# Optimization experiments

Hardware: AMD Instinct MI355X
Metric: run time of the kernel (lower is better)

The kernel has to match this reference:

```python
import jax, jax.numpy as jnp
import numpy as np

H = 16         # num query heads
KV = 8         # num kv heads
HD = 64        # head_dim
WINDOW = 512   # sliding window size
ROPE_BASE = 10000.0


def rotate_half(x):
    x1, x2 = x[..., : x.shape[-1] // 2], x[..., x.shape[-1] // 2 :]
    return jnp.concatenate((-x2, x1), axis=-1)


def rope_cos_sin(seq_len, dim, dtype):
    inv_freq = 1.0 / (ROPE_BASE ** (jnp.arange(0, dim, 2, dtype=jnp.float32) / dim))
    t = jnp.arange(seq_len, dtype=jnp.float32)
    freqs = jnp.outer(t, inv_freq)              # [S, dim/2]
    emb = jnp.concatenate((freqs, freqs), axis=-1)  # [S, dim]
    return jnp.cos(emb).astype(dtype), jnp.sin(emb).astype(dtype)


def setup_inputs() -> dict:
    key = jax.random.key(0)
    ks = jax.random.split(key, 5)
    B, S, D = 2, 2048, 1024
    std = 0.02
    return {
        "hidden_states": jax.random.normal(ks[0], (B, S, D), dtype=jnp.float32),
        "Wq": jax.random.normal(ks[1], (D, H * HD), dtype=jnp.float32) * std,
        "Wk": jax.random.normal(ks[2], (D, KV * HD), dtype=jnp.float32) * std,
        "Wv": jax.random.normal(ks[3], (D, KV * HD), dtype=jnp.float32) * std,
        "Wo": jax.random.normal(ks[4], (H * HD, D), dtype=jnp.float32) * std,
    }


def reference(hidden_states, Wq, Wk, Wv, Wo):
    B, S, D = hidden_states.shape
    n_rep = H // KV

    q = (hidden_states @ Wq).reshape(B, S, H, HD).transpose(0, 2, 1, 3)   # [B,H,S,hd]
    k = (hidden_states @ Wk).reshape(B, S, KV, HD).transpose(0, 2, 1, 3)  # [B,KV,S,hd]
    v = (hidden_states @ Wv).reshape(B, S, KV, HD).transpose(0, 2, 1, 3)

    cos, sin = rope_cos_sin(S, HD, q.dtype)  # [S,hd]
    cos = cos[None, None]
    sin = sin[None, None]
    q = q * cos + rotate_half(q) * sin
    k = k * cos + rotate_half(k) * sin

    # repeat kv heads for GQA ([:, :, None] expand + reshape == repeat along head axis)
    k = jnp.repeat(k, n_rep, axis=1)  # [B,H,S,hd]
    v = jnp.repeat(v, n_rep, axis=1)

    scores = jnp.einsum("bhqd,bhkd->bhqk", q, k) / jnp.sqrt(jnp.asarray(HD, q.dtype))
    i = jnp.arange(S)[:, None]
    j = jnp.arange(S)[None, :]
    allowed = (j <= i) & (j >= i - WINDOW)  # causal + sliding window
    scores = jnp.where(allowed[None, None], scores, -jnp.inf)

    attn = jax.nn.softmax(scores, axis=-1)
    out = jnp.einsum("bhqk,bhkd->bhqd", attn, v)          # [B,H,S,hd]
    out = out.transpose(0, 2, 1, 3).reshape(B, S, H * HD)  # [B,S,D]
    return out @ Wo
```

## Files before the change

### kernel.cpp

```cpp
#include <hip/hip_runtime.h>
#include <hip/hip_bf16.h>

typedef __attribute__((ext_vector_type(8))) short short8;
typedef __attribute__((ext_vector_type(4))) float f32x4;

#define S_LEN 2048
#define NH 16
#define NKV 8
#define HD 64
#define WIN 512
#define DMODEL 1024
#define LOG2_10000 13.287712379549449f

#define GLOAD16(g, l)                                                        \
    __builtin_amdgcn_global_load_lds(                                        \
        (const __attribute__((address_space(1))) unsigned int*)(g),          \
        (__attribute__((address_space(3))) unsigned int*)(l), 16, 0, 0)

__global__ void cast_bf16_kernel(const float* __restrict__ X,
                                 __hip_bfloat16* __restrict__ Y, int n) {
    int i = (blockIdx.x * 256 + threadIdx.x) * 4;
    if (i + 3 < n) {
        float4 v = *reinterpret_cast<const float4*>(X + i);
        Y[i + 0] = __float2bfloat16(v.x);
        Y[i + 1] = __float2bfloat16(v.y);
        Y[i + 2] = __float2bfloat16(v.z);
        Y[i + 3] = __float2bfloat16(v.w);
    }
}

__global__ void transpose_cast4_kernel(const float* __restrict__ W0,
                                       const float* __restrict__ W1,
                                       const float* __restrict__ W2,
                                       const float* __restrict__ W3,
                                       __hip_bfloat16* __restrict__ WqkvT,
                                       __hip_bfloat16* __restrict__ WoT) {
    __shared__ float tile[32][33];
    const int K = DMODEL;
    const float* W;
    __hip_bfloat16* WT;
    int N;
    switch (blockIdx.z) {
        case 0: W = W0; WT = WqkvT;                          N = 1024; break;
        case 1: W = W1; WT = WqkvT + (size_t)1024 * K;       N = 512;  break;
        case 2: W = W2; WT = WqkvT + (size_t)1536 * K;       N = 512;  break;
        default: W = W3; WT = WoT;                           N = 1024; break;
    }
    if ((int)blockIdx.x * 32 >= N) return;
    int nx = blockIdx.x * 32 + threadIdx.x;
    int k0 = blockIdx.y * 32;
#pragma unroll
    for (int r = 0; r < 4; ++r) {
        int k = k0 + threadIdx.y + r * 8;
        tile[threadIdx.y + r * 8][threadIdx.x] = W[(size_t)k * N + nx];
    }
    __syncthreads();
#pragma unroll
    for (int r = 0; r < 4; ++r) {
        int nn = blockIdx.x * 32 + threadIdx.y + r * 8;
        int kk = k0 + threadIdx.x;
        WT[(size_t)nn * K + kk] = __float2bfloat16(tile[threadIdx.x][threadIdx.y + r * 8]);
    }
}

template <int MODE>
__global__ __launch_bounds__(256) void gemm256_kernel(
    const __hip_bfloat16* __restrict__ A,
    const __hip_bfloat16* __restrict__ BT,
    void* __restrict__ o0, void* __restrict__ o1, void* __restrict__ o2,
    int N, int K) {
    __shared__ __hip_bfloat16 ldsA[128 * 32];
    __shared__ __hip_bfloat16 ldsB[128 * 32];
    const int tx = threadIdx.x;
    const int wave = tx >> 6;
    const int lane = tx & 63;
    const int l16 = lane & 15;
    const int quad = lane >> 4;
    const int col0 = blockIdx.x * 128;
    const int row0 = blockIdx.y * 128;
    const int wrow = (wave >> 1) * 64;
    const int wcol = (wave & 1) * 64;

    f32x4 acc[4][4] = {};

    const int arow = tx >> 2;
    const int kc8 = (tx & 3) * 8;
    const __hip_bfloat16* gA = A + (size_t)(row0 + arow) * K + kc8;
    const __hip_bfloat16* gB = BT + (size_t)(col0 + arow) * K + kc8;
    char* lA = (char*)ldsA + tx * 16;
    char* lB = (char*)ldsB + tx * 16;

    for (int k0 = 0; k0 < K; k0 += 32) {
        GLOAD16(gA + k0, lA);
        GLOAD16(gA + (size_t)64 * K + k0, lA + 4096);
        GLOAD16(gB + k0, lB);
        GLOAD16(gB + (size_t)64 * K + k0, lB + 4096);
        __syncthreads();
        short8 af[4], bf[4];
#pragma unroll
        for (int i = 0; i < 4; ++i) {
            af[i] = *reinterpret_cast<const short8*>(
                ldsA + (wrow + i * 16 + l16) * 32 + quad * 8);
            bf[i] = *reinterpret_cast<const short8*>(
                ldsB + (wcol + i * 16 + l16) * 32 + quad * 8);
        }
#pragma unroll
        for (int mi = 0; mi < 4; ++mi)
#pragma unroll
            for (int ni = 0; ni < 4; ++ni)
                acc[mi][ni] = __builtin_amdgcn_mfma_f32_16x16x32_bf16(
                    af[mi], bf[ni], acc[mi][ni], 0, 0, 0);
        __syncthreads();
    }

    const int rbase = row0 + wrow;
    if (MODE == 0) {
        const int cbaseg = col0 + wcol;
        const bool isQ = (cbaseg < DMODEL);
        const bool isK = (cbaseg >= DMODEL) && (cbaseg < DMODEL + 512);
        if (isQ || isK) {
            float invf[2];
            invf[0] = exp2f(-(float)(l16)      * (LOG2_10000 / 32.0f));
            invf[1] = exp2f(-(float)(16 + l16) * (LOG2_10000 / 32.0f));
#pragma unroll
            for (int mi = 0; mi < 4; ++mi)
#pragma unroll
                for (int r = 0; r < 4; ++r) {
                    int srow = (rbase + mi * 16 + quad * 4 + r) & (S_LEN - 1);
#pragma unroll
                    for (int ni = 0; ni < 2; ++ni) {
                        float ang = (float)srow * invf[ni];
                        float c = __cosf(ang), s = __sinf(ang);
                        float x1 = acc[mi][ni][r], x2 = acc[mi][ni + 2][r];
                        acc[mi][ni][r]     = x1 * c - x2 * s;
                        acc[mi][ni + 2][r] = x2 * c + x1 * s;
                    }
                }
            __hip_bfloat16* Co = (__hip_bfloat16*)(isQ ? o0 : o1);
            int cbase = isQ ? cbaseg : cbaseg - DMODEL;
            int rowstride = isQ ? (NH * HD) : (NKV * HD);
#pragma unroll
            for (int mi = 0; mi < 4; ++mi)
#pragma unroll
                for (int ni = 0; ni < 4; ++ni) {
                    size_t col = cbase + ni * 16 + l16;
#pragma unroll
                    for (int r = 0; r < 4; ++r)
                        Co[(size_t)(rbase + mi * 16 + quad * 4 + r) * rowstride + col] =
                            __float2bfloat16(acc[mi][ni][r]);
                }
        } else {
            __hip_bfloat16* VTo = (__hip_bfloat16*)o2;
            int bb = row0 >> 11;
#pragma unroll
            for (int mi = 0; mi < 4; ++mi) {
                int s = ((rbase + mi * 16 + quad * 4) & (S_LEN - 1));
#pragma unroll
                for (int ni = 0; ni < 4; ++ni) {
                    int colv = cbaseg - 1536 + ni * 16 + l16;
                    int vh = colv >> 6, d = colv & 63;
                    alignas(8) __hip_bfloat16 hv[4];
#pragma unroll
                    for (int r = 0; r < 4; ++r) hv[r] = __float2bfloat16(acc[mi][ni][r]);
                    *reinterpret_cast<ushort4*>(
                        VTo + ((size_t)(bb * NKV + vh) * HD + d) * S_LEN + s) =
                        *reinterpret_cast<ushort4*>(hv);
                }
            }
        }
    } else {
        float* Co = (float*)o0;
#pragma unroll
        for (int mi = 0; mi < 4; ++mi)
#pragma unroll
            for (int ni = 0; ni < 4; ++ni) {
                size_t col = col0 + wcol + ni * 16 + l16;
#pragma unroll
                for (int r = 0; r < 4; ++r)
                    Co[(size_t)(rbase + mi * 16 + quad * 4 + r) * N + col] = acc[mi][ni][r];
            }
    }
}

__global__ __launch_bounds__(256) void attn_mfma_kernel(
    const __hip_bfloat16* __restrict__ Q,
    const __hip_bfloat16* __restrict__ K,
    const __hip_bfloat16* __restrict__ VT,
    __hip_bfloat16* __restrict__ O) {
    __shared__ __hip_bfloat16 ldsK[2][64][64];
    __shared__ __hip_bfloat16 ldsVT[2][64][64];
    __shared__ __hip_bfloat16 ldsP[4][16][80];
    const int tx = threadIdx.x;
    const int wave = tx >> 6;
    const int lane = tx & 63;
    const int l16 = lane & 15;
    const int quad = lane >> 4;
    const int q0 = blockIdx.x * 64;
    const int h = blockIdx.y;
    const int b = blockIdx.z;
    const int kvh = h >> 1;
    const int qi = q0 + wave * 16 + l16;

    short8 aq0, aq1;
    {
        const __hip_bfloat16* qp =
            Q + (size_t)(b * S_LEN + qi) * (NH * HD) + h * HD + quad * 8;
        aq0 = *reinterpret_cast<const short8*>(qp);
        aq1 = *reinterpret_cast<const short8*>(qp + 32);
    }
    f32x4 acc_o[4] = {};
    float m = -1e30f, l = 0.f;
    const float SL2 = 0.125f * 1.4426950408889634f;

    const int s_row = tx >> 3;
    const int s_c8 = (((tx & 7) ^ (s_row & 7))) * 8;
    const int sw = (l16 & 7);
    auto stage = [&](int j0, int bf) {
        char* lk = (char*)(&ldsK[bf][0][0]) + tx * 16;
        char* lv = (char*)(&ldsVT[bf][0][0]) + tx * 16;
#pragma unroll
        for (int r = 0; r < 2; ++r) {
            int row = s_row + r * 32;
            GLOAD16(K + (size_t)(b * S_LEN + j0 + row) * (NKV * HD) + kvh * HD + s_c8,
                    lk + r * 4096);
            GLOAD16(VT + ((size_t)(b * NKV + kvh) * HD + row) * S_LEN + j0 + s_c8,
                    lv + r * 4096);
        }
    };

    const int kstart = (q0 >= WIN) ? (q0 - WIN) : 0;
    stage(kstart, 0);
    int buf = 0;

    for (int j0 = kstart; j0 <= q0; j0 += 64) {
        __syncthreads();
        if (j0 + 64 <= q0) stage(j0 + 64, buf ^ 1);

        f32x4 sacc[4] = {};
#pragma unroll
        for (int t = 0; t < 4; ++t) {
            const __hip_bfloat16* krow = &ldsK[buf][t * 16 + l16][0];
            short8 bk0 = *reinterpret_cast<const short8*>(krow + ((quad ^ sw) * 8));
            short8 bk1 = *reinterpret_cast<const short8*>(krow + (((4 + quad) ^ sw) * 8));
            sacc[t] = __builtin_amdgcn_mfma_f32_16x16x32_bf16(bk0, aq0, sacc[t], 0, 0, 0);
            sacc[t] = __builtin_amdgcn_mfma_f32_16x16x32_bf16(bk1, aq1, sacc[t], 0, 0, 0);
        }

        float sv[4][4];
        const bool need_mask = (j0 == q0) || (q0 >= WIN && j0 == kstart);
        if (need_mask) {
#pragma unroll
            for (int t = 0; t < 4; ++t)
#pragma unroll
                for (int r = 0; r < 4; ++r) {
                    int j = j0 + t * 16 + quad * 4 + r;
                    bool ok = (j <= qi) && (j + WIN >= qi);
                    sv[t][r] = ok ? sacc[t][r] * SL2 : -1e30f;
                }
        } else {
#pragma unroll
            for (int t = 0; t < 4; ++t)
#pragma unroll
                for (int r = 0; r < 4; ++r) sv[t][r] = sacc[t][r] * SL2;
        }

        float cm = -1e30f;
#pragma unroll
        for (int t = 0; t < 4; ++t)
#pragma unroll
            for (int r = 0; r < 4; ++r) cm = fmaxf(cm, sv[t][r]);
        cm = fmaxf(cm, __shfl_xor(cm, 16));
        cm = fmaxf(cm, __shfl_xor(cm, 32));
        float mn = fmaxf(m, cm);
        float alpha = exp2f(m - mn);
        m = mn;
        float sp = 0.f;
#pragma unroll
        for (int t = 0; t < 4; ++t)
#pragma unroll
            for (int r = 0; r < 4; ++r) { sv[t][r] = exp2f(sv[t][r] - mn); sp += sv[t][r]; }
        sp += __shfl_xor(sp, 16);
        sp += __shfl_xor(sp, 32);
        l = l * alpha + sp;
#pragma unroll
        for (int t = 0; t < 4; ++t)
#pragma unroll
            for (int r = 0; r < 4; ++r) acc_o[t][r] *= alpha;

#pragma unroll
        for (int t = 0; t < 4; ++t) {
            alignas(8) __hip_bfloat16 hp[4];
#pragma unroll
            for (int r = 0; r < 4; ++r) hp[r] = __float2bfloat16(sv[t][r]);
            *reinterpret_cast<ushort4*>(&ldsP[wave][l16][t * 16 + quad * 4]) =
                *reinterpret_cast<ushort4*>(hp);
        }
#pragma unroll
        for (int ks = 0; ks < 2; ++ks) {
            short8 pf = *reinterpret_cast<const short8*>(&ldsP[wave][l16][ks * 32 + quad * 8]);
#pragma unroll
            for (int t = 0; t < 4; ++t) {
                const __hip_bfloat16* vrow = &ldsVT[buf][t * 16 + l16][0];
                short8 vf = *reinterpret_cast<const short8*>(
                    vrow + (((ks * 4 + quad) ^ sw) * 8));
                acc_o[t] = __builtin_amdgcn_mfma_f32_16x16x32_bf16(vf, pf, acc_o[t], 0, 0, 0);
            }
        }
        buf ^= 1;
    }

    float inv = 1.f / l;
    __hip_bfloat16* op = O + (size_t)(b * S_LEN + qi) * (NH * HD) + h * HD;
#pragma unroll
    for (int t = 0; t < 4; ++t) {
        alignas(8) __hip_bfloat16 ho[4];
#pragma unroll
        for (int r = 0; r < 4; ++r) ho[r] = __float2bfloat16(acc_o[t][r] * inv);
        *reinterpret_cast<ushort4*>(op + t * 16 + quad * 4) =
            *reinterpret_cast<ushort4*>(ho);
    }
}

extern "C" void kernel_launch(void* const* d_in, const int* in_sizes, int n_in,
                              void* d_out, int out_size, void* d_ws, size_t ws_size,
                              hipStream_t stream) {
    const float* X  = (const float*)d_in[0];
    const float* Wq = (const float*)d_in[1];
    const float* Wk = (const float*)d_in[2];
    const float* Wv = (const float*)d_in[3];
    const float* Wo = (const float*)d_in[4];
    float* out = (float*)d_out;

    const int ROWS = 2 * S_LEN;
    char* ws = (char*)d_ws;
    size_t off = 0;
    __hip_bfloat16* Xb     = (__hip_bfloat16*)(ws + off); off += (size_t)ROWS * DMODEL * 2;
    __hip_bfloat16* WqkvT  = (__hip_bfloat16*)(ws + off); off += (size_t)2048 * DMODEL * 2;
    __hip_bfloat16* WoT    = (__hip_bfloat16*)(ws + off); off += (size_t)DMODEL * DMODEL * 2;
    __hip_bfloat16* Qb     = (__hip_bfloat16*)(ws + off); off += (size_t)ROWS * (NH * HD) * 2;
    __hip_bfloat16* Kb     = (__hip_bfloat16*)(ws + off); off += (size_t)ROWS * (NKV * HD) * 2;
    __hip_bfloat16* VTg    = (__hip_bfloat16*)(ws + off); off += (size_t)ROWS * (NKV * HD) * 2;
    __hip_bfloat16* Ob     = (__hip_bfloat16*)(ws + off); off += (size_t)ROWS * (NH * HD) * 2;

    cast_bf16_kernel<<<(ROWS * DMODEL) / (256 * 4), 256, 0, stream>>>(X, Xb, ROWS * DMODEL);
    transpose_cast4_kernel<<<dim3(32, 32, 4), dim3(32, 8), 0, stream>>>(
        Wq, Wk, Wv, Wo, WqkvT, WoT);

    gemm256_kernel<0><<<dim3(2048 / 128, ROWS / 128), 256, 0, stream>>>(
        Xb, WqkvT, Qb, Kb, VTg, 2048, DMODEL);

    attn_mfma_kernel<<<dim3(S_LEN / 64, NH, 2), 256, 0, stream>>>(Qb, Kb, VTg, Ob);

    gemm256_kernel<1><<<dim3(DMODEL / 128, ROWS / 128), 256, 0, stream>>>(
        Ob, WoT, out, nullptr, nullptr, DMODEL, DMODEL);
}
```

Baseline: 174.7 us.

## Process both GQA query heads per block to share K/V tile loads

Each attention block now handles the two query heads that share one KV head, so each staged K and V^T tile feeds twice the MFMA work. The grid shrinks from 16 to 8 heads along y, halving global K/V traffic and LDS staging per query. It also raises the launch-bounds occupancy hint to 3 blocks per CU. In exchange register pressure roughly doubles for accumulators and Q fragments, the grid has half as many blocks (512), and the larger P scratch buffer uses more LDS.

```diff
diff --git a/kernel.cpp b/kernel.cpp
--- a/kernel.cpp
+++ b/kernel.cpp
@@ -182,34 +182,34 @@
     }
 }
 
-__global__ __launch_bounds__(256) void attn_mfma_kernel(
+__global__ __launch_bounds__(256, 3) void attn_mfma_kernel(
     const __hip_bfloat16* __restrict__ Q,
     const __hip_bfloat16* __restrict__ K,
     const __hip_bfloat16* __restrict__ VT,
     __hip_bfloat16* __restrict__ O) {
     __shared__ __hip_bfloat16 ldsK[2][64][64];
     __shared__ __hip_bfloat16 ldsVT[2][64][64];
-    __shared__ __hip_bfloat16 ldsP[4][16][80];
+    __shared__ __hip_bfloat16 ldsP[4][2][16][80];
     const int tx = threadIdx.x;
     const int wave = tx >> 6;
     const int lane = tx & 63;
     const int l16 = lane & 15;
     const int quad = lane >> 4;
     const int q0 = blockIdx.x * 64;
-    const int h = blockIdx.y;
+    const int kvh = blockIdx.y;
     const int b = blockIdx.z;
-    const int kvh = h >> 1;
     const int qi = q0 + wave * 16 + l16;
 
-    short8 aq0, aq1;
-    {
+    short8 aq[2][2];
+#pragma unroll
+    for (int hh = 0; hh < 2; ++hh) {
         const __hip_bfloat16* qp =
-            Q + (size_t)(b * S_LEN + qi) * (NH * HD) + h * HD + quad * 8;
-        aq0 = *reinterpret_cast<const short8*>(qp);
-        aq1 = *reinterpret_cast<const short8*>(qp + 32);
-    }
-    f32x4 acc_o[4] = {};
-    float m = -1e30f, l = 0.f;
+            Q + (size_t)(b * S_LEN + qi) * (NH * HD) + (2 * kvh + hh) * HD + quad * 8;
+        aq[hh][0] = *reinterpret_cast<const short8*>(qp);
+        aq[hh][1] = *reinterpret_cast<const short8*>(qp + 32);
+    }
+    f32x4 acc_o[2][4] = {};
+    float m[2] = {-1e30f, -1e30f}, l[2] = {0.f, 0.f};
     const float SL2 = 0.125f * 1.4426950408889634f;
 
     const int s_row = tx >> 3;
@@ -236,88 +236,100 @@
         __syncthreads();
         if (j0 + 64 <= q0) stage(j0 + 64, buf ^ 1);
 
-        f32x4 sacc[4] = {};
+        f32x4 sacc[2][4] = {};
 #pragma unroll
         for (int t = 0; t < 4; ++t) {
             const __hip_bfloat16* krow = &ldsK[buf][t * 16 + l16][0];
             short8 bk0 = *reinterpret_cast<const short8*>(krow + ((quad ^ sw) * 8));
             short8 bk1 = *reinterpret_cast<const short8*>(krow + (((4 + quad) ^ sw) * 8));
-            sacc[t] = __builtin_amdgcn_mfma_f32_16x16x32_bf16(bk0, aq0, sacc[t], 0, 0, 0);
-            sacc[t] = __builtin_amdgcn_mfma_f32_16x16x32_bf16(bk1, aq1, sacc[t], 0, 0, 0);
-        }
-
-        float sv[4][4];
+            sacc[0][t] = __builtin_amdgcn_mfma_f32_16x16x32_bf16(bk0, aq[0][0], sacc[0][t], 0, 0, 0);
+            sacc[0][t] = __builtin_amdgcn_mfma_f32_16x16x32_bf16(bk1, aq[0][1], sacc[0][t], 0, 0, 0);
+            sacc[1][t] = __builtin_amdgcn_mfma_f32_16x16x32_bf16(bk0, aq[1][0], sacc[1][t], 0, 0, 0);
+            sacc[1][t] = __builtin_amdgcn_mfma_f32_16x16x32_bf16(bk1, aq[1][1], sacc[1][t], 0, 0, 0);
+        }
+
         const bool need_mask = (j0 == q0) || (q0 >= WIN && j0 == kstart);
-        if (need_mask) {
+#pragma unroll
+        for (int hh = 0; hh < 2; ++hh) {
+            float sv[4][4];
+            if (need_mask) {
+#pragma unroll
+                for (int t = 0; t < 4; ++t)
+#pragma unroll
+                    for (int r = 0; r < 4; ++r) {
+                        int j = j0 + t * 16 + quad * 4 + r;
+                        bool ok = (j <= qi) && (j + WIN >= qi);
+                        sv[t][r] = ok ? sacc[hh][t][r] * SL2 : -1e30f;
+                    }
+            } else {
+#pragma unroll
+                for (int t = 0; t < 4; ++t)
+#pragma unroll
+                    for (int r = 0; r < 4; ++r) sv[t][r] = sacc[hh][t][r] * SL2;
+            }
+            float cm = -1e30f;
 #pragma unroll
             for (int t = 0; t < 4; ++t)
 #pragma unroll
-                for (int r = 0; r < 4; ++r) {
-                    int j = j0 + t * 16 + quad * 4 + r;
-                    bool ok = (j <= qi) && (j + WIN >= qi);
-                    sv[t][r] = ok ? sacc[t][r] * SL2 : -1e30f;
-                }
-        } else {
+                for (int r = 0; r < 4; ++r) cm = fmaxf(cm, sv[t][r]);
+            cm = fmaxf(cm, __shfl_xor(cm, 16));
+            cm = fmaxf(cm, __shfl_xor(cm, 32));
+            float mn = fmaxf(m[hh], cm);
+            float alpha = exp2f(m[hh] - mn);
+            m[hh] = mn;
+            float sp = 0.f;
 #pragma unroll
             for (int t = 0; t < 4; ++t)
 #pragma unroll
-                for (int r = 0; r < 4; ++r) sv[t][r] = sacc[t][r] * SL2;
-        }
-
-        float cm = -1e30f;
-#pragma unroll
-        for (int t = 0; t < 4; ++t)
-#pragma unroll
-            for (int r = 0; r < 4; ++r) cm = fmaxf(cm, sv[t][r]);
-        cm = fmaxf(cm, __shfl_xor(cm, 16));
-        cm = fmaxf(cm, __shfl_xor(cm, 32));
-        float mn = fmaxf(m, cm);
-        float alpha = exp2f(m - mn);
-        m = mn;
-        float sp = 0.f;
-#pragma unroll
-        for (int t = 0; t < 4; ++t)
-#pragma unroll
-            for (int r = 0; r < 4; ++r) { sv[t][r] = exp2f(sv[t][r] - mn); sp += sv[t][r]; }
-        sp += __shfl_xor(sp, 16);
-        sp += __shfl_xor(sp, 32);
-        l = l * alpha + sp;
-#pragma unroll
-        for (int t = 0; t < 4; ++t)
-#pragma unroll
-            for (int r = 0; r < 4; ++r) acc_o[t][r] *= alpha;
-
-#pragma unroll
-        for (int t = 0; t < 4; ++t) {
-            alignas(8) __hip_bfloat16 hp[4];
-#pragma unroll
-            for (int r = 0; r < 4; ++r) hp[r] = __float2bfloat16(sv[t][r]);
-            *reinterpret_cast<ushort4*>(&ldsP[wave][l16][t * 16 + quad * 4]) =
-                *reinterpret_cast<ushort4*>(hp);
-        }
+                for (int r = 0; r < 4; ++r) { sv[t][r] = exp2f(sv[t][r] - mn); sp += sv[t][r]; }
+            sp += __shfl_xor(sp, 16);
+            sp += __shfl_xor(sp, 32);
+            l[hh] = l[hh] * alpha + sp;
+#pragma unroll
+            for (int t = 0; t < 4; ++t)
+#pragma unroll
+                for (int r = 0; r < 4; ++r) acc_o[hh][t][r] *= alpha;
+#pragma unroll
+            for (int t = 0; t < 4; ++t) {
+                alignas(8) __hip_bfloat16 hp[4];
+#pragma unroll
+                for (int r = 0; r < 4; ++r) hp[r] = __float2bfloat16(sv[t][r]);
+                *reinterpret_cast<ushort4*>(&ldsP[wave][hh][l16][t * 16 + quad * 4]) =
+                    *reinterpret_cast<ushort4*>(hp);
+            }
+        }
+
 #pragma unroll
         for (int ks = 0; ks < 2; ++ks) {
-            short8 pf = *reinterpret_cast<const short8*>(&ldsP[wave][l16][ks * 32 + quad * 8]);
+            short8 pf0 = *reinterpret_cast<const short8*>(
+                &ldsP[wave][0][l16][ks * 32 + quad * 8]);
+            short8 pf1 = *reinterpret_cast<const short8*>(
+                &ldsP[wave][1][l16][ks * 32 + quad * 8]);
 #pragma unroll
             for (int t = 0; t < 4; ++t) {
                 const __hip_bfloat16* vrow = &ldsVT[buf][t * 16 + l16][0];
                 short8 vf = *reinterpret_cast<const short8*>(
                     vrow + (((ks * 4 + quad) ^ sw) * 8));
-                acc_o[t] = __builtin_amdgcn_mfma_f32_16x16x32_bf16(vf, pf, acc_o[t], 0, 0, 0);
+                acc_o[0][t] = __builtin_amdgcn_mfma_f32_16x16x32_bf16(vf, pf0, acc_o[0][t], 0, 0, 0);
+                acc_o[1][t] = __builtin_amdgcn_mfma_f32_16x16x32_bf16(vf, pf1, acc_o[1][t], 0, 0, 0);
             }
         }
         buf ^= 1;
     }
 
-    float inv = 1.f / l;
-    __hip_bfloat16* op = O + (size_t)(b * S_LEN + qi) * (NH * HD) + h * HD;
-#pragma unroll
-    for (int t = 0; t < 4; ++t) {
-        alignas(8) __hip_bfloat16 ho[4];
-#pragma unroll
-        for (int r = 0; r < 4; ++r) ho[r] = __float2bfloat16(acc_o[t][r] * inv);
-        *reinterpret_cast<ushort4*>(op + t * 16 + quad * 4) =
-            *reinterpret_cast<ushort4*>(ho);
+#pragma unroll
+    for (int hh = 0; hh < 2; ++hh) {
+        float inv = 1.f / l[hh];
+        __hip_bfloat16* op =
+            O + (size_t)(b * S_LEN + qi) * (NH * HD) + (2 * kvh + hh) * HD;
+#pragma unroll
+        for (int t = 0; t < 4; ++t) {
+            alignas(8) __hip_bfloat16 ho[4];
+#pragma unroll
+            for (int r = 0; r < 4; ++r) ho[r] = __float2bfloat16(acc_o[hh][t][r] * inv);
+            *reinterpret_cast<ushort4*>(op + t * 16 + quad * 4) =
+                *reinterpret_cast<ushort4*>(ho);
+        }
     }
 }
 
@@ -349,7 +361,7 @@
     gemm256_kernel<0><<<dim3(2048 / 128, ROWS / 128), 256, 0, stream>>>(
         Xb, WqkvT, Qb, Kb, VTg, 2048, DMODEL);
 
-    attn_mfma_kernel<<<dim3(S_LEN / 64, NH, 2), 256, 0, stream>>>(Qb, Kb, VTg, Ob);
+    attn_mfma_kernel<<<dim3(S_LEN / 64, NKV, 2), 256, 0, stream>>>(Qb, Kb, VTg, Ob);
 
     gemm256_kernel<1><<<dim3(DMODEL / 128, ROWS / 128), 256, 0, stream>>>(
         Ob, WoT, out, nullptr, nullptr, DMODEL, DMODEL);
```

After: 174.9 us. Within noise of the previous version (+0.1%).
